# Kernel tuning notes

Measured on AMD Instinct MI355X. Metric: run time of the kernel, lower is better.

## Reference

```python
import jax, jax.numpy as jnp
import numpy as np

B, N, M, C, NR = 8, 2048, 512, 256, 4  # batch, unknown pts, known pts, feat channels, rotation anchors
MLP = [512, 256, 256]
EPS_D, EPS_BN = 1e-8, 1e-5


def setup_inputs() -> dict:
    key = jax.random.key(0)
    ks = jax.random.split(key, 10)
    inp = {
        "unknown": jax.random.normal(ks[0], (B, N, 3), jnp.float32),
        "known": jax.random.normal(ks[1], (B, M, 3), jnp.float32),
        "unknow_feats": jax.random.normal(ks[2], (B, C, NR, N), jnp.float32),
        "known_feats": jax.random.normal(ks[3], (B, C, NR, M), jnp.float32),
    }
    # SharedMLP params: Conv2d 1x1 (no bias since bn=True) + BN gamma/beta per layer
    inp["W1"] = jax.random.normal(ks[4], (MLP[1], MLP[0]), jnp.float32) * (1.0 / np.sqrt(MLP[0]))
    inp["g1"] = jnp.ones((MLP[1],), jnp.float32)
    inp["b1"] = jnp.zeros((MLP[1],), jnp.float32)
    inp["W2"] = jax.random.normal(ks[5], (MLP[2], MLP[1]), jnp.float32) * (1.0 / np.sqrt(MLP[1]))
    inp["g2"] = jnp.ones((MLP[2],), jnp.float32)
    inp["b2"] = jnp.zeros((MLP[2],), jnp.float32)
    return inp


def _conv_bn_relu(x, W, g, b):
    # x: (B, Cin, Nr, n); 1x1 conv == channel GEMM; BN in training mode (batch stats)
    y = jnp.einsum("oi,birn->born", W, x)
    mean = jnp.mean(y, axis=(0, 2, 3), keepdims=True)
    var = jnp.var(y, axis=(0, 2, 3), keepdims=True)
    y = (y - mean) * jax.lax.rsqrt(var + EPS_BN)
    y = y * g[None, :, None, None] + b[None, :, None, None]
    return jax.nn.relu(y)


def reference(unknown, known, unknow_feats, known_feats, W1, g1, b1, W2, g2, b2):
    b_, c1, nr, n = unknow_feats.shape
    c2 = known_feats.shape[1]
    m = known_feats.shape[3]
    # --- 3-NN search: squared distances (B, n, m) ---
    d2 = (jnp.sum(unknown ** 2, -1, keepdims=True)
          + jnp.sum(known ** 2, -1)[:, None, :]
          - 2.0 * jnp.einsum("bnd,bmd->bnm", unknown, known))
    neg_top, idx = jax.lax.top_k(-d2, 3)          # (B, n, 3)
    dist2 = jnp.maximum(-neg_top, 0.0)
    # --- inverse-distance weights ---
    dist_recip = 1.0 / (jnp.sqrt(dist2) + EPS_D)
    weight = dist_recip / jnp.sum(dist_recip, axis=2, keepdims=True)  # (B, n, 3)
    # --- gather + weighted interpolation ---
    feats = known_feats.reshape(b_, c2 * nr, m).transpose(0, 2, 1)    # (B, m, C2*Nr)
    nn_features = jax.vmap(lambda f, i: f[i])(feats, idx)             # (B, n, 3, C2*Nr)
    interp = jnp.sum(weight[..., None] * nn_features, axis=2)         # (B, n, C2*Nr)
    interp = interp.transpose(0, 2, 1).reshape(b_, c2, nr, n)
    # --- concat skip + SharedMLP ---
    x = jnp.concatenate([interp, unknow_feats], axis=1)               # (B, C1+C2, Nr, n)
    x = _conv_bn_relu(x, W1, g1, b1)
    x = _conv_bn_relu(x, W2, g2, b2)
    return x
```

## Files before the change

kernel.cpp:

```cpp
#include <hip/hip_runtime.h>
#include <math.h>

#define B_   8
#define N_   2048
#define M_   512
#define C_   256
#define NR_  4
#define J_   8192
#define CIN1 512
#define BN_CNT 65536.0f
#define NSLICE 512

using f16   = _Float16;
using f16x2 = __attribute__((ext_vector_type(2))) _Float16;
using f16x8 = __attribute__((ext_vector_type(8))) _Float16;
using f32x4 = __attribute__((ext_vector_type(4))) float;

#define KNN_INSERT(e, j)                                              \
  do {                                                                \
    if ((e) < d0)      { d2v = d1; i2 = i1; d1 = d0; i1 = i0; d0 = (e); i0 = (j); } \
    else if ((e) < d1) { d2v = d1; i2 = i1; d1 = (e); i1 = (j); }     \
    else if ((e) < d2v){ d2v = (e); i2 = (j); }                       \
  } while (0)

__global__ __launch_bounds__(256) void knn_kernel(
    const float* __restrict__ unknown, const float* __restrict__ known,
    int* __restrict__ idx_out, float* __restrict__ w_out)
{
  __shared__ float4 kp[M_];
  const int b = blockIdx.y;
  const int t = threadIdx.x;
  for (int i = t; i < M_; i += 256) {
    const float kx = known[(b * M_ + i) * 3 + 0];
    const float ky = known[(b * M_ + i) * 3 + 1];
    const float kz = known[(b * M_ + i) * 3 + 2];
    kp[(i & 63) * 8 + (i >> 6)] = make_float4(kx, ky, kz, kx * kx + ky * ky + kz * kz);
  }
  __syncthreads();

  const int p = t >> 3;
  const int s = t & 7;
  const int n = blockIdx.x * 32 + p;
  const float ux = unknown[(b * N_ + n) * 3 + 0];
  const float uy = unknown[(b * N_ + n) * 3 + 1];
  const float uz = unknown[(b * N_ + n) * 3 + 2];
  const float un2 = ux * ux + uy * uy + uz * uz;

  float d0 = 3.4e38f, d1 = 3.4e38f, d2v = 3.4e38f;
  int i0 = 0, i1 = 0, i2 = 0;
#pragma unroll 8
  for (int it = 0; it < 64; ++it) {
    const float4 k4 = kp[it * 8 + s];
    const int m = s * 64 + it;
    const float d = (un2 + k4.w) - 2.0f * (ux * k4.x + uy * k4.y + uz * k4.z);
    KNN_INSERT(d, m);
  }
#pragma unroll
  for (int off = 1; off < 8; off <<= 1) {
    const float e0 = __shfl_xor(d0, off), e1 = __shfl_xor(d1, off), e2 = __shfl_xor(d2v, off);
    const int   j0 = __shfl_xor(i0, off), j1 = __shfl_xor(i1, off), j2 = __shfl_xor(i2, off);
    KNN_INSERT(e0, j0);
    KNN_INSERT(e1, j1);
    KNN_INSERT(e2, j2);
  }
  if (s == 0) {
    const float r0 = 1.0f / (sqrtf(fmaxf(d0, 0.f)) + 1e-8f);
    const float r1 = 1.0f / (sqrtf(fmaxf(d1, 0.f)) + 1e-8f);
    const float r2 = 1.0f / (sqrtf(fmaxf(d2v, 0.f)) + 1e-8f);
    const float rs = r0 + r1 + r2;
    const int base = (b * N_ + n) * 3;
    idx_out[base + 0] = i0; idx_out[base + 1] = i1; idx_out[base + 2] = i2;
    w_out[base + 0] = r0 / rs; w_out[base + 1] = r1 / rs; w_out[base + 2] = r2 / rs;
  }
}

__global__ __launch_bounds__(256) void prep_kernel(
    const float* __restrict__ kf, const int* __restrict__ idx,
    const float* __restrict__ wgt, f16* __restrict__ x16,
    const float* __restrict__ uf, f16* __restrict__ uf16)
{
  if (blockIdx.y < 64) {
    const int n0 = (blockIdx.x * 256 + threadIdx.x) * 2;
    const int c0 = blockIdx.y * 4;
    const int b = blockIdx.z >> 2, r = blockIdx.z & 3;
    const int ba = (b * N_ + n0) * 3;
    const int ia0 = idx[ba + 0], ia1 = idx[ba + 1], ia2 = idx[ba + 2];
    const int ib0 = idx[ba + 3], ib1 = idx[ba + 4], ib2 = idx[ba + 5];
    const float wa0 = wgt[ba + 0], wa1 = wgt[ba + 1], wa2 = wgt[ba + 2];
    const float wb0 = wgt[ba + 3], wb1 = wgt[ba + 4], wb2 = wgt[ba + 5];
#pragma unroll
    for (int cc = 0; cc < 4; ++cc) {
      const int c = c0 + cc;
      const float* row = kf + (((size_t)b * C_ + c) * NR_ + r) * M_;
      f16x2 v;
      v[0] = (f16)(wa0 * row[ia0] + wa1 * row[ia1] + wa2 * row[ia2]);
      v[1] = (f16)(wb0 * row[ib0] + wb1 * row[ib1] + wb2 * row[ib2]);
      *(f16x2*)&x16[(((size_t)b * C_ + c) * NR_ + r) * N_ + n0] = v;
    }
  } else {
    const size_t u = ((size_t)(blockIdx.z * 32 + (blockIdx.y - 64)) * 4 + blockIdx.x) * 256 + threadIdx.x;
    const size_t e = u * 16;
    const float4 a0 = *(const float4*)&uf[e + 0];
    const float4 a1 = *(const float4*)&uf[e + 4];
    const float4 a2 = *(const float4*)&uf[e + 8];
    const float4 a3 = *(const float4*)&uf[e + 12];
    f16x8 v0, v1;
    v0[0] = (f16)a0.x; v0[1] = (f16)a0.y; v0[2] = (f16)a0.z; v0[3] = (f16)a0.w;
    v0[4] = (f16)a1.x; v0[5] = (f16)a1.y; v0[6] = (f16)a1.z; v0[7] = (f16)a1.w;
    v1[0] = (f16)a2.x; v1[1] = (f16)a2.y; v1[2] = (f16)a2.z; v1[3] = (f16)a2.w;
    v1[4] = (f16)a3.x; v1[5] = (f16)a3.y; v1[6] = (f16)a3.z; v1[7] = (f16)a3.w;
    *(f16x8*)&uf16[e + 0] = v0;
    *(f16x8*)&uf16[e + 8] = v1;
  }
}

__global__ __launch_bounds__(256) void cvt_w_kernel(
    const float* __restrict__ W1, const float* __restrict__ W2,
    f16* __restrict__ w1h, f16* __restrict__ w2h)
{
  const int i = blockIdx.x * 256 + threadIdx.x;
  if (i < 256 * 512) w1h[i] = (f16)W1[i];
  if (i < 256 * 256) w2h[i] = (f16)W2[i];
}

template <int K, bool G2>
__global__ __launch_bounds__(256, 2) void mfma_gemm(
    const f16* __restrict__ Wf,
    const f16* __restrict__ Xh, const f16* __restrict__ Xh2,
    const float* __restrict__ sc, const float* __restrict__ sh,
    f16* __restrict__ Yh,
    float* __restrict__ psum, float* __restrict__ psq)
{
  __shared__ __align__(16) f16 Ws[128][40];
  __shared__ __align__(16) f16 Xs[256][40];
  const int t = threadIdx.x;
  const int l = t & 63, w = t >> 6;
  const int wm = w >> 1, wn = w & 1;
  const int g = l >> 4, ln = l & 15;
  const int jb = blockIdx.x * 256;
  const int ob = blockIdx.y * 128;
  const int b  = blockIdx.z;

  const int wo0 = t >> 2, wkg = (t & 3) * 8;
  const int xn0 = (t & 127) * 2;
  const int xcc0 = t >> 7;
  const int s0 = t & 127, s1 = 128 + (t & 127);
  const int xswz = t & 3;

  f32x4 acc[4][8];
#pragma unroll
  for (int i = 0; i < 4; ++i)
#pragma unroll
    for (int j = 0; j < 8; ++j) acc[i][j] = (f32x4){0.f, 0.f, 0.f, 0.f};

  f16x8 wr[2];
  f16x2 xr[2][8];

  auto prefetch = [&](int kb_) {
#pragma unroll
    for (int it = 0; it < 2; ++it) {
      wr[it] = *(const f16x8*)&Wf[(size_t)(ob + it * 64 + wo0) * K + kb_ + wkg];
      const int kk = kb_ + (xcc0 + it * 2) * 8;
      const f16* src;
      if constexpr (!G2)
        src = (kk < C_) ? Xh + ((size_t)b * C_ + kk) * J_
                        : Xh2 + ((size_t)b * C_ + (kk - C_)) * J_;
      else
        src = Xh + ((size_t)b * C_ + kk) * J_;
      src += jb + xn0;
#pragma unroll
      for (int i = 0; i < 8; ++i) xr[it][i] = *(const f16x2*)&src[(size_t)i * J_];
    }
  };

  auto store_lds = [&](int kb_) {
#pragma unroll
    for (int it = 0; it < 2; ++it) {
      *(f16x8*)&Ws[it * 64 + wo0][wkg] = wr[it];
      const int cc = xcc0 + it * 2;
      const int col = (cc ^ xswz) * 8;
      f16x8 v0, v1;
      if constexpr (G2) {
        const int kk = kb_ + cc * 8;
#pragma unroll
        for (int i = 0; i < 8; ++i) {
          const float scv = sc[kk + i], shv = sh[kk + i];
          v0[i] = (f16)fmaxf((float)xr[it][i][0] * scv + shv, 0.f);
          v1[i] = (f16)fmaxf((float)xr[it][i][1] * scv + shv, 0.f);
        }
      } else {
#pragma unroll
        for (int i = 0; i < 8; ++i) { v0[i] = xr[it][i][0]; v1[i] = xr[it][i][1]; }
      }
      *(f16x8*)&Xs[s0][col] = v0;
      *(f16x8*)&Xs[s1][col] = v1;
    }
  };

  prefetch(0);
  for (int kb = 0; kb < K; kb += 32) {
    store_lds(kb);
    __syncthreads();
    if (kb + 32 < K) prefetch(kb + 32);

    f16x8 af[4], bf[8];
#pragma unroll
    for (int f = 0; f < 4; ++f)
      af[f] = *(const f16x8*)&Ws[wm * 64 + f * 16 + ln][g * 8];
#pragma unroll
    for (int f = 0; f < 8; ++f) {
      const int sg = (ln & 1) * 128 + wn * 64 + f * 8 + (ln >> 1);
      bf[f] = *(const f16x8*)&Xs[sg][(g ^ (sg & 3)) * 8];
    }
#pragma unroll
    for (int fm = 0; fm < 4; ++fm)
#pragma unroll
      for (int fn = 0; fn < 8; ++fn)
        acc[fm][fn] = __builtin_amdgcn_mfma_f32_16x16x32_f16(af[fm], bf[fn], acc[fm][fn], 0, 0, 0);
    __syncthreads();
  }

  const int slice2 = (b * 32 + blockIdx.x) * 2 + wn;
#pragma unroll
  for (int fm = 0; fm < 4; ++fm) {
#pragma unroll
    for (int r = 0; r < 4; ++r) {
      const int o = ob + wm * 64 + fm * 16 + g * 4 + r;
      float s = 0.f, q = 0.f;
#pragma unroll
      for (int fn = 0; fn < 8; ++fn) {
        const float v = acc[fm][fn][r];
        const int j = jb + wn * 128 + fn * 16 + ln;
        Yh[((size_t)b * C_ + o) * J_ + j] = (f16)v;
        s += v; q += v * v;
      }
#pragma unroll
      for (int off = 1; off < 16; off <<= 1) {
        s += __shfl_xor(s, off);
        q += __shfl_xor(q, off);
      }
      if (ln == 0) {
        psum[(size_t)slice2 * C_ + o] = s;
        psq [(size_t)slice2 * C_ + o] = q;
      }
    }
  }
}

__global__ __launch_bounds__(256) void finalize_bn(
    const float* __restrict__ psum, const float* __restrict__ psq,
    const float* __restrict__ g, const float* __restrict__ bt,
    float* __restrict__ sc, float* __restrict__ sh)
{
  const int c = blockIdx.x, t = threadIdx.x;
  float s = 0.f, q = 0.f;
  for (int s2 = t; s2 < NSLICE; s2 += 256) {
    s += psum[(size_t)s2 * C_ + c];
    q += psq [(size_t)s2 * C_ + c];
  }
#pragma unroll
  for (int off = 1; off < 64; off <<= 1) {
    s += __shfl_xor(s, off);
    q += __shfl_xor(q, off);
  }
  __shared__ float ls[4], lq[4];
  if ((t & 63) == 0) { ls[t >> 6] = s; lq[t >> 6] = q; }
  __syncthreads();
  if (t == 0) {
    s = ls[0] + ls[1] + ls[2] + ls[3];
    q = lq[0] + lq[1] + lq[2] + lq[3];
    const float mean = s / BN_CNT;
    const float var = q / BN_CNT - mean * mean;
    const float rstd = rsqrtf(var + 1e-5f);
    const float scale = g[c] * rstd;
    sc[c] = scale;
    sh[c] = bt[c] - mean * scale;
  }
}

__global__ __launch_bounds__(256) void bn_relu_kernel(
    const f16* __restrict__ y2, float* __restrict__ out,
    const float* __restrict__ sc, const float* __restrict__ sh)
{
  const size_t i8 = (size_t)blockIdx.x * 256 + threadIdx.x;
  const int c = (int)((i8 >> 10) & (C_ - 1));
  const float s = sc[c], h = sh[c];
  const f16x8 v = *(const f16x8*)&y2[i8 * 8];
  float4 o0, o1;
  o0.x = fmaxf((float)v[0] * s + h, 0.f);
  o0.y = fmaxf((float)v[1] * s + h, 0.f);
  o0.z = fmaxf((float)v[2] * s + h, 0.f);
  o0.w = fmaxf((float)v[3] * s + h, 0.f);
  o1.x = fmaxf((float)v[4] * s + h, 0.f);
  o1.y = fmaxf((float)v[5] * s + h, 0.f);
  o1.z = fmaxf((float)v[6] * s + h, 0.f);
  o1.w = fmaxf((float)v[7] * s + h, 0.f);
  ((float4*)out)[i8 * 2]     = o0;
  ((float4*)out)[i8 * 2 + 1] = o1;
}

extern "C" void kernel_launch(void* const* d_in, const int* in_sizes, int n_in,
                              void* d_out, int out_size, void* d_ws, size_t ws_size,
                              hipStream_t stream)
{
  const float* unknown = (const float*)d_in[0];
  const float* known   = (const float*)d_in[1];
  const float* uf      = (const float*)d_in[2];
  const float* kf      = (const float*)d_in[3];
  const float* W1      = (const float*)d_in[4];
  const float* g1      = (const float*)d_in[5];
  const float* b1      = (const float*)d_in[6];
  const float* W2      = (const float*)d_in[7];
  const float* g2      = (const float*)d_in[8];
  const float* b2      = (const float*)d_in[9];
  float* out = (float*)d_out;

  float* wsf = (float*)d_ws;
  int*   idx   = (int*)d_ws;
  float* wgt   = wsf + 49152;
  float* sc1   = wsf + 98304;
  float* sh1   = wsf + 98560;
  float* sc2   = wsf + 98816;
  float* sh2   = wsf + 99072;
  float* p1s   = wsf + 99328;
  float* p1q   = wsf + 230400;
  float* p2s   = wsf + 361472;
  float* p2q   = wsf + 492544;
  f16*   w1h   = (f16*)(wsf + 623616);
  f16*   w2h   = (f16*)(wsf + 689152);
  f16*   x16   = (f16*)(wsf + 721920);
  f16*   y2h   = x16;
  f16*   y1h   = (f16*)d_out;
  f16*   uf16  = (f16*)d_out + 16777216;

  cvt_w_kernel<<<512, 256, 0, stream>>>(W1, W2, w1h, w2h);
  knn_kernel<<<dim3(N_ / 32, B_), 256, 0, stream>>>(unknown, known, idx, wgt);
  prep_kernel<<<dim3(4, 96, 32), 256, 0, stream>>>(kf, idx, wgt, x16, uf, uf16);

  mfma_gemm<CIN1, false><<<dim3(32, 2, 8), 256, 0, stream>>>(
      w1h, x16, uf16, nullptr, nullptr, y1h, p1s, p1q);
  finalize_bn<<<256, 256, 0, stream>>>(p1s, p1q, g1, b1, sc1, sh1);

  mfma_gemm<C_, true><<<dim3(32, 2, 8), 256, 0, stream>>>(
      w2h, y1h, nullptr, sc1, sh1, y2h, p2s, p2q);
  finalize_bn<<<256, 256, 0, stream>>>(p2s, p2q, g2, b2, sc2, sh2);

  bn_relu_kernel<<<8192, 256, 0, stream>>>(y2h, out, sc2, sh2);
}
```

Before: 273.4 us.

## Fuse skip-feature fp16 conversion into first GEMM and stage known rows in LDS

Removes the separate pass that converted unknow_feats to fp16. The first GEMM now reads the fp32 skip features directly and converts them while staging into shared memory, which saves a full write and re-read of a 16M-element intermediate. The interpolation kernel now loads the four known-feature rows into shared memory before gathering, replacing scattered global reads. In exchange, the GEMM reads twice the bytes per element for the skip half and its prefetch path gains branches.

New measurement: 244.4 us. 10.6% less time.

```diff
diff --git a/kernel.cpp b/kernel.cpp
--- a/kernel.cpp
+++ b/kernel.cpp
@@ -74,43 +74,34 @@
   }
 }
 
-__global__ __launch_bounds__(256) void prep_kernel(
+__global__ __launch_bounds__(256) void interp_kernel(
     const float* __restrict__ kf, const int* __restrict__ idx,
-    const float* __restrict__ wgt, f16* __restrict__ x16,
-    const float* __restrict__ uf, f16* __restrict__ uf16)
-{
-  if (blockIdx.y < 64) {
-    const int n0 = (blockIdx.x * 256 + threadIdx.x) * 2;
-    const int c0 = blockIdx.y * 4;
-    const int b = blockIdx.z >> 2, r = blockIdx.z & 3;
-    const int ba = (b * N_ + n0) * 3;
-    const int ia0 = idx[ba + 0], ia1 = idx[ba + 1], ia2 = idx[ba + 2];
-    const int ib0 = idx[ba + 3], ib1 = idx[ba + 4], ib2 = idx[ba + 5];
-    const float wa0 = wgt[ba + 0], wa1 = wgt[ba + 1], wa2 = wgt[ba + 2];
-    const float wb0 = wgt[ba + 3], wb1 = wgt[ba + 4], wb2 = wgt[ba + 5];
-#pragma unroll
-    for (int cc = 0; cc < 4; ++cc) {
-      const int c = c0 + cc;
-      const float* row = kf + (((size_t)b * C_ + c) * NR_ + r) * M_;
-      f16x2 v;
-      v[0] = (f16)(wa0 * row[ia0] + wa1 * row[ia1] + wa2 * row[ia2]);
-      v[1] = (f16)(wb0 * row[ib0] + wb1 * row[ib1] + wb2 * row[ib2]);
-      *(f16x2*)&x16[(((size_t)b * C_ + c) * NR_ + r) * N_ + n0] = v;
-    }
-  } else {
-    const size_t u = ((size_t)(blockIdx.z * 32 + (blockIdx.y - 64)) * 4 + blockIdx.x) * 256 + threadIdx.x;
-    const size_t e = u * 16;
-    const float4 a0 = *(const float4*)&uf[e + 0];
-    const float4 a1 = *(const float4*)&uf[e + 4];
-    const float4 a2 = *(const float4*)&uf[e + 8];
-    const float4 a3 = *(const float4*)&uf[e + 12];
-    f16x8 v0, v1;
-    v0[0] = (f16)a0.x; v0[1] = (f16)a0.y; v0[2] = (f16)a0.z; v0[3] = (f16)a0.w;
-    v0[4] = (f16)a1.x; v0[5] = (f16)a1.y; v0[6] = (f16)a1.z; v0[7] = (f16)a1.w;
-    v1[0] = (f16)a2.x; v1[1] = (f16)a2.y; v1[2] = (f16)a2.z; v1[3] = (f16)a2.w;
-    v1[4] = (f16)a3.x; v1[5] = (f16)a3.y; v1[6] = (f16)a3.z; v1[7] = (f16)a3.w;
-    *(f16x8*)&uf16[e + 0] = v0;
-    *(f16x8*)&uf16[e + 8] = v1;
+    const float* __restrict__ wgt, f16* __restrict__ out)
+{
+  __shared__ float rows[4][M_];
+  const int t = threadIdx.x;
+  const int c0 = blockIdx.y * 4;
+  const int b = blockIdx.z >> 2, r = blockIdx.z & 3;
+#pragma unroll
+  for (int cc = 0; cc < 4; ++cc) {
+    const float* src = kf + (((size_t)b * C_ + c0 + cc) * NR_ + r) * M_;
+#pragma unroll
+    for (int u = 0; u < 2; ++u) rows[cc][u * 256 + t] = src[u * 256 + t];
+  }
+  __syncthreads();
+
+  const int n0 = (blockIdx.x * 256 + t) * 2;
+  const int ba = (b * N_ + n0) * 3;
+  const int ia0 = idx[ba + 0], ia1 = idx[ba + 1], ia2 = idx[ba + 2];
+  const int ib0 = idx[ba + 3], ib1 = idx[ba + 4], ib2 = idx[ba + 5];
+  const float wa0 = wgt[ba + 0], wa1 = wgt[ba + 1], wa2 = wgt[ba + 2];
+  const float wb0 = wgt[ba + 3], wb1 = wgt[ba + 4], wb2 = wgt[ba + 5];
+#pragma unroll
+  for (int cc = 0; cc < 4; ++cc) {
+    f16x2 v;
+    v[0] = (f16)(wa0 * rows[cc][ia0] + wa1 * rows[cc][ia1] + wa2 * rows[cc][ia2]);
+    v[1] = (f16)(wb0 * rows[cc][ib0] + wb1 * rows[cc][ib1] + wb2 * rows[cc][ib2]);
+    *(f16x2*)&out[(((size_t)b * C_ + c0 + cc) * NR_ + r) * N_ + n0] = v;
   }
 }
 
@@ -126,7 +117,7 @@
 template <int K, bool G2>
 __global__ __launch_bounds__(256, 2) void mfma_gemm(
     const f16* __restrict__ Wf,
-    const f16* __restrict__ Xh, const f16* __restrict__ Xh2,
+    const f16* __restrict__ Xh, const float* __restrict__ Xf,
     const float* __restrict__ sc, const float* __restrict__ sh,
     f16* __restrict__ Yh,
     float* __restrict__ psum, float* __restrict__ psq)
@@ -154,22 +145,28 @@
     for (int j = 0; j < 8; ++j) acc[i][j] = (f32x4){0.f, 0.f, 0.f, 0.f};
 
   f16x8 wr[2];
-  f16x2 xr[2][8];
+  uint2 xr[2][8];
 
   auto prefetch = [&](int kb_) {
 #pragma unroll
     for (int it = 0; it < 2; ++it) {
       wr[it] = *(const f16x8*)&Wf[(size_t)(ob + it * 64 + wo0) * K + kb_ + wkg];
       const int kk = kb_ + (xcc0 + it * 2) * 8;
-      const f16* src;
-      if constexpr (!G2)
-        src = (kk < C_) ? Xh + ((size_t)b * C_ + kk) * J_
-                        : Xh2 + ((size_t)b * C_ + (kk - C_)) * J_;
-      else
-        src = Xh + ((size_t)b * C_ + kk) * J_;
-      src += jb + xn0;
-#pragma unroll
-      for (int i = 0; i < 8; ++i) xr[it][i] = *(const f16x2*)&src[(size_t)i * J_];
+      if constexpr (!G2) {
+        if (kk < C_) {
+          const f16* src = Xh + ((size_t)b * C_ + kk) * J_ + jb + xn0;
+#pragma unroll
+          for (int i = 0; i < 8; ++i) xr[it][i].x = *(const unsigned int*)&src[(size_t)i * J_];
+        } else {
+          const float* src = Xf + ((size_t)b * C_ + (kk - C_)) * J_ + jb + xn0;
+#pragma unroll
+          for (int i = 0; i < 8; ++i) xr[it][i] = *(const uint2*)&src[(size_t)i * J_];
+        }
+      } else {
+        const f16* src = Xh + ((size_t)b * C_ + kk) * J_ + jb + xn0;
+#pragma unroll
+        for (int i = 0; i < 8; ++i) xr[it][i].x = *(const unsigned int*)&src[(size_t)i * J_];
+      }
     }
   };
 
@@ -184,13 +181,23 @@
         const int kk = kb_ + cc * 8;
 #pragma unroll
         for (int i = 0; i < 8; ++i) {
+          const f16x2 pr = __builtin_bit_cast(f16x2, xr[it][i].x);
           const float scv = sc[kk + i], shv = sh[kk + i];
-          v0[i] = (f16)fmaxf((float)xr[it][i][0] * scv + shv, 0.f);
-          v1[i] = (f16)fmaxf((float)xr[it][i][1] * scv + shv, 0.f);
+          v0[i] = (f16)fmaxf((float)pr[0] * scv + shv, 0.f);
+          v1[i] = (f16)fmaxf((float)pr[1] * scv + shv, 0.f);
+        }
+      } else if (kb_ < C_) {
+#pragma unroll
+        for (int i = 0; i < 8; ++i) {
+          const f16x2 pr = __builtin_bit_cast(f16x2, xr[it][i].x);
+          v0[i] = pr[0]; v1[i] = pr[1];
         }
       } else {
 #pragma unroll
-        for (int i = 0; i < 8; ++i) { v0[i] = xr[it][i][0]; v1[i] = xr[it][i][1]; }
+        for (int i = 0; i < 8; ++i) {
+          const float2 pr = __builtin_bit_cast(float2, xr[it][i]);
+          v0[i] = (f16)pr.x; v1[i] = (f16)pr.y;
+        }
       }
       *(f16x8*)&Xs[s0][col] = v0;
       *(f16x8*)&Xs[s1][col] = v1;
@@ -331,14 +338,13 @@
   f16*   x16   = (f16*)(wsf + 721920);
   f16*   y2h   = x16;
   f16*   y1h   = (f16*)d_out;
-  f16*   uf16  = (f16*)d_out + 16777216;
 
   cvt_w_kernel<<<512, 256, 0, stream>>>(W1, W2, w1h, w2h);
   knn_kernel<<<dim3(N_ / 32, B_), 256, 0, stream>>>(unknown, known, idx, wgt);
-  prep_kernel<<<dim3(4, 96, 32), 256, 0, stream>>>(kf, idx, wgt, x16, uf, uf16);
+  interp_kernel<<<dim3(4, 64, 32), 256, 0, stream>>>(kf, idx, wgt, x16);
 
   mfma_gemm<CIN1, false><<<dim3(32, 2, 8), 256, 0, stream>>>(
-      w1h, x16, uf16, nullptr, nullptr, y1h, p1s, p1q);
+      w1h, x16, uf, nullptr, nullptr, y1h, p1s, p1q);
   finalize_bn<<<256, 256, 0, stream>>>(p1s, p1q, g1, b1, sc1, sh1);
 
   mfma_gemm<C_, true><<<dim3(32, 2, 8), 256, 0, stream>>>(
```
